# Performance work log

Hardware: AMD Instinct MI355X
Metric: run time of the kernel (lower is better)

## Reference

```python
import jax, jax.numpy as jnp
import numpy as np

B, S, E, D, A = 64, 1024, 512, 512, 512

def setup_inputs() -> dict:
    key = jax.random.key(0)
    ks = jax.random.split(key, 12)
    xavier = lambda k, shape: jax.random.uniform(k, shape, jnp.float32,
        -jnp.sqrt(6.0 / (shape[0] + shape[1])), jnp.sqrt(6.0 / (shape[0] + shape[1])))
    return {
        "encoder_states": jax.random.normal(ks[0], (B, S, E), jnp.float32),
        "decoder_state": jax.random.normal(ks[1], (B, D), jnp.float32),
        "encoder_mask": jnp.ones((B, S), jnp.int32),
        "coverage": jax.random.uniform(ks[2], (B, S), jnp.float32),
        # learned parameters (torch nn.Linear: y = x @ W.T + b)
        "W_enc": xavier(ks[3], (A, E)),           # encoder_projection, no bias
        "W_dec": xavier(ks[4], (A, D)),           # decoder_projection, no bias
        "w_attn": xavier(ks[5], (1, A)),          # attention_weight, no bias
        "W_layer1": xavier(ks[6], (A, A)),        # attention_layers[0]
        "b_layer1": jnp.zeros((A,), jnp.float32),
        "W_cov": xavier(ks[7], (A, 1)),           # coverage_projection, no bias
        "W_gate": xavier(ks[8], (A, E + D)),      # gate Linear
        "b_gate": jnp.zeros((A,), jnp.float32),
    }


def reference(encoder_states, decoder_state, encoder_mask, coverage,
              W_enc, W_dec, w_attn, W_layer1, b_layer1, W_cov, W_gate, b_gate):
    # projections
    proj_enc = jnp.einsum('bse,ae->bsa', encoder_states, W_enc)        # [B,S,A]
    proj_dec = jnp.einsum('bd,ad->ba', decoder_state, W_dec)[:, None]  # [B,1,A]
    attn_in = proj_enc + proj_dec
    # coverage: Linear(1->A) on coverage[..., None]
    attn_in = attn_in + coverage[..., None] * W_cov[None, None, :, 0]  # [B,S,A]
    feats = jnp.tanh(attn_in)
    # extra residual tanh layer (num_layers=2 -> one layer)
    feats = jnp.tanh(jnp.einsum('bsa,ca->bsc', feats, W_layer1) + b_layer1 + feats)
    scores = jnp.einsum('bsa,a->bs', feats, w_attn[0])                 # [B,S]
    scores = jnp.where(encoder_mask == 0, -1e9, scores)
    attn_w = jax.nn.softmax(scores, axis=-1)                           # [B,S]
    context = jnp.einsum('bs,bse->be', attn_w, encoder_states)         # [B,E]
    # gating
    gate_in = jnp.concatenate([context, decoder_state], axis=-1)       # [B,E+D]
    gate = jax.nn.sigmoid(jnp.einsum('bf,af->ba', gate_in, W_gate) + b_gate)
    context = gate * context
    updated_coverage = coverage + attn_w
    return (context, attn_w, updated_coverage)
```

## Files before the change

kernel.cpp:

```cpp
#include <hip/hip_runtime.h>
#include <hip/hip_bf16.h>

typedef unsigned short ushort_t;
typedef __attribute__((ext_vector_type(8))) short short8;
typedef __attribute__((ext_vector_type(4))) float float4_t;
typedef __attribute__((ext_vector_type(2))) float float2_t;
typedef __attribute__((ext_vector_type(4))) unsigned int uint4_t;

#define BB 64
#define SS 1024
#define EE 512
#define DD 512
#define AA 512
#define MM (BB*SS)
#define KK 512
#define BM 128
#define BN 128
#define BK 32
#define BKP 40
#define BK2 64

__device__ __forceinline__ float bf2f(ushort_t u) {
    return __uint_as_float(((unsigned int)u) << 16);
}
__device__ __forceinline__ ushort_t f2bf(float f) {
    unsigned int u = __float_as_uint(f);
    unsigned int r = u + 0x7fffu + ((u >> 16) & 1u);
    return (ushort_t)(r >> 16);
}
__device__ __forceinline__ float ldmix(int f32, const void* p, long idx) {
    return f32 ? ((const float*)p)[idx] : bf2f(((const ushort_t*)p)[idx]);
}
__device__ __forceinline__ void stmix(int f32, void* p, long idx, float v) {
    if (f32) ((float*)p)[idx] = v;
    else     ((ushort_t*)p)[idx] = f2bf(v);
}
__device__ __forceinline__ float fast_tanh(float x) {
    float e = __expf(2.f * x);
    return 1.f - 2.f / (e + 1.f);
}
__device__ __forceinline__ void glds16(const ushort_t* g, ushort_t* l) {
    typedef __attribute__((address_space(1))) const void gas_t;
    typedef __attribute__((address_space(3))) void las_t;
    gas_t* gp = (gas_t*)g;
    las_t* lp = (las_t*)l;
    __builtin_amdgcn_global_load_lds(gp, lp, 16, 0, 0);
}

__global__ void k_detect(const ushort_t* __restrict__ enc, int* __restrict__ flag) {
    __shared__ int cnt;
    int tid = threadIdx.x;
    if (tid == 0) cnt = 0;
    __syncthreads();
    int c = 0;
    const uint4_t* p = (const uint4_t*)enc;
    for (int i = tid; i < 4096; i += 256) {
        uint4_t v = p[i];
        #pragma unroll
        for (int j = 0; j < 4; j++) {
            unsigned int u = v[j];
            if (((u >> 7) & 0xFFu) == 0xFFu || ((u >> 23) & 0xFFu) == 0xFFu) c++;
        }
    }
    atomicAdd(&cnt, c);
    __syncthreads();
    if (tid == 0) *flag = (cnt > 0) ? 1 : 0;
}

__global__ __launch_bounds__(256)
void k_conv_w(const void* __restrict__ Wenc, const void* __restrict__ W1,
              const int* __restrict__ flagp,
              ushort_t* __restrict__ WencB, ushort_t* __restrict__ W1B) {
    const int f32 = *flagp;
    const void* src = blockIdx.y ? W1 : Wenc;
    ushort_t* dst = blockIdx.y ? W1B : WencB;
    long e0 = ((long)blockIdx.x * 256 + threadIdx.x) * 8;
    short8 p;
    #pragma unroll
    for (int j = 0; j < 8; j++) p[j] = (short)f2bf(ldmix(f32, src, e0 + j));
    *(short8*)&dst[e0] = p;
}

__global__ __launch_bounds__(256)
void k_conv_enc(const void* __restrict__ enc, const int* __restrict__ flagp,
                ushort_t* __restrict__ out) {
    if (*flagp == 0) return;
    const float4_t* src = (const float4_t*)enc;
    size_t i0 = (size_t)blockIdx.x * 256 + threadIdx.x;
    size_t n8 = (size_t)MM * EE / 8;
    size_t stride = (size_t)gridDim.x * 256;
    for (size_t i = i0; i < n8; i += stride) {
        float4_t v0 = src[2 * i], v1 = src[2 * i + 1];
        short8 p;
        p[0] = (short)f2bf(v0[0]); p[1] = (short)f2bf(v0[1]);
        p[2] = (short)f2bf(v0[2]); p[3] = (short)f2bf(v0[3]);
        p[4] = (short)f2bf(v1[0]); p[5] = (short)f2bf(v1[1]);
        p[6] = (short)f2bf(v1[2]); p[7] = (short)f2bf(v1[3]);
        *(short8*)&out[i * 8] = p;
    }
}

__global__ __launch_bounds__(256)
void k_proj_dec(const void* __restrict__ dec,
                const void* __restrict__ Wdec,
                const int* __restrict__ flagp,
                float* __restrict__ proj) {
    __shared__ float x[DD];
    const int f32 = *flagp;
    const int b = blockIdx.y;
    const int tid = threadIdx.x, lane = tid & 63, wave = tid >> 6;
    x[tid]       = ldmix(f32, dec, (long)b * DD + tid);
    x[tid + 256] = ldmix(f32, dec, (long)b * DD + tid + 256);
    __syncthreads();
    const int a = blockIdx.x * 4 + wave;
    float s = 0.f;
    if (f32) {
        const float* wr = (const float*)Wdec + (size_t)a * DD + lane * 8;
        #pragma unroll
        for (int j = 0; j < 8; j++) s += wr[j] * x[lane * 8 + j];
    } else {
        const ushort_t* wr = (const ushort_t*)Wdec + (size_t)a * DD + lane * 8;
        short8 w = *(const short8*)wr;
        #pragma unroll
        for (int j = 0; j < 8; j++) s += bf2f((ushort_t)w[j]) * x[lane * 8 + j];
    }
    #pragma unroll
    for (int off = 1; off < 64; off <<= 1) s += __shfl_xor(s, off);
    if (lane == 0) proj[b * AA + a] = s;
}

__device__ __forceinline__ void stage8(int f32, const void* g, long row, int col,
                                       ushort_t* lds) {
    if (f32) {
        const float* gf = (const float*)g + row * KK + col;
        float4_t v0 = *(const float4_t*)(gf);
        float4_t v1 = *(const float4_t*)(gf + 4);
        short8 p;
        p[0] = (short)f2bf(v0[0]); p[1] = (short)f2bf(v0[1]);
        p[2] = (short)f2bf(v0[2]); p[3] = (short)f2bf(v0[3]);
        p[4] = (short)f2bf(v1[0]); p[5] = (short)f2bf(v1[1]);
        p[6] = (short)f2bf(v1[2]); p[7] = (short)f2bf(v1[3]);
        *(short8*)lds = p;
    } else {
        const ushort_t* gb = (const ushort_t*)g + row * KK + col;
        *(short8*)lds = *(const short8*)gb;
    }
}

__global__ __launch_bounds__(256)
void k_gemm1(const void* __restrict__ Xg,
             const void* __restrict__ Bg,
             const float* __restrict__ proj_dec,
             const void* __restrict__ cov,
             const void* __restrict__ Wcov,
             const int* __restrict__ flagp,
             ushort_t* __restrict__ feats) {
    __shared__ ushort_t As[BM * BKP];
    __shared__ ushort_t Bs[BN * BKP];
    const int f32 = *flagp;
    const int tid = threadIdx.x;
    const int lane = tid & 63, wave = tid >> 6;
    const int quad = lane >> 4, l16 = lane & 15;
    const int wm = wave >> 1, wn = wave & 1;
    const int m0 = blockIdx.y * BM, n0 = blockIdx.x * BN;

    float4_t acc[4][4];
    #pragma unroll
    for (int i = 0; i < 4; i++)
        #pragma unroll
        for (int j = 0; j < 4; j++) acc[i][j] = (float4_t){0.f, 0.f, 0.f, 0.f};

    const int srow = lane >> 2;
    const int scol = (lane & 3) * 8;
    ushort_t* lA0 = &As[(wave * 32 + srow) * BKP + scol];
    ushort_t* lB0 = &Bs[(wave * 32 + srow) * BKP + scol];

    for (int kt = 0; kt < KK; kt += BK) {
        __syncthreads();
        stage8(f32, Xg, (long)(m0 + wave * 32 + srow), kt + scol, lA0);
        stage8(f32, Xg, (long)(m0 + wave * 32 + srow + 16), kt + scol, lA0 + 16 * BKP);
        stage8(f32, Bg, (long)(n0 + wave * 32 + srow), kt + scol, lB0);
        stage8(f32, Bg, (long)(n0 + wave * 32 + srow + 16), kt + scol, lB0 + 16 * BKP);
        __syncthreads();
        short8 af[4], bfr[4];
        #pragma unroll
        for (int mt = 0; mt < 4; mt++)
            af[mt] = *(const short8*)&As[(wm * 64 + mt * 16 + l16) * BKP + quad * 8];
        #pragma unroll
        for (int nt = 0; nt < 4; nt++)
            bfr[nt] = *(const short8*)&Bs[(wn * 64 + nt * 16 + l16) * BKP + quad * 8];
        #pragma unroll
        for (int mt = 0; mt < 4; mt++)
            #pragma unroll
            for (int nt = 0; nt < 4; nt++)
                acc[mt][nt] = __builtin_amdgcn_mfma_f32_16x16x32_bf16(af[mt], bfr[nt], acc[mt][nt], 0, 0, 0);
    }

    #pragma unroll
    for (int mt = 0; mt < 4; mt++) {
        #pragma unroll
        for (int r = 0; r < 4; r++) {
            int m = m0 + wm * 64 + mt * 16 + quad * 4 + r;
            int b = m >> 10;
            float covv = ldmix(f32, cov, m);
            #pragma unroll
            for (int nt = 0; nt < 4; nt++) {
                int n = n0 + wn * 64 + nt * 16 + l16;
                float v = acc[mt][nt][r] + proj_dec[b * AA + n] + covv * ldmix(f32, Wcov, n);
                feats[(size_t)m * AA + n] = f2bf(fast_tanh(v));
            }
        }
    }
}

__global__ __launch_bounds__(256)
void k_gemm2(const ushort_t* __restrict__ Xg,
             const void* __restrict__ Bg,
             const void* __restrict__ b1,
             const void* __restrict__ wattn,
             const int* __restrict__ flagp,
             float* __restrict__ scores) {
    __shared__ ushort_t As[BM * BKP];
    __shared__ ushort_t Bs[BN * BKP];
    const int f32 = *flagp;
    const int tid = threadIdx.x;
    const int lane = tid & 63, wave = tid >> 6;
    const int quad = lane >> 4, l16 = lane & 15;
    const int wm = wave >> 1, wn = wave & 1;
    const int m0 = blockIdx.y * BM, n0 = blockIdx.x * BN;

    float4_t acc[4][4];
    #pragma unroll
    for (int i = 0; i < 4; i++)
        #pragma unroll
        for (int j = 0; j < 4; j++) acc[i][j] = (float4_t){0.f, 0.f, 0.f, 0.f};

    const int srow = lane >> 2;
    const int scol = (lane & 3) * 8;
    ushort_t* lA0 = &As[(wave * 32 + srow) * BKP + scol];
    ushort_t* lB0 = &Bs[(wave * 32 + srow) * BKP + scol];

    for (int kt = 0; kt < KK; kt += BK) {
        __syncthreads();
        stage8(0,   Xg, (long)(m0 + wave * 32 + srow), kt + scol, lA0);
        stage8(0,   Xg, (long)(m0 + wave * 32 + srow + 16), kt + scol, lA0 + 16 * BKP);
        stage8(f32, Bg, (long)(n0 + wave * 32 + srow), kt + scol, lB0);
        stage8(f32, Bg, (long)(n0 + wave * 32 + srow + 16), kt + scol, lB0 + 16 * BKP);
        __syncthreads();
        short8 af[4], bfr[4];
        #pragma unroll
        for (int mt = 0; mt < 4; mt++)
            af[mt] = *(const short8*)&As[(wm * 64 + mt * 16 + l16) * BKP + quad * 8];
        #pragma unroll
        for (int nt = 0; nt < 4; nt++)
            bfr[nt] = *(const short8*)&Bs[(wn * 64 + nt * 16 + l16) * BKP + quad * 8];
        #pragma unroll
        for (int mt = 0; mt < 4; mt++)
            #pragma unroll
            for (int nt = 0; nt < 4; nt++)
                acc[mt][nt] = __builtin_amdgcn_mfma_f32_16x16x32_bf16(af[mt], bfr[nt], acc[mt][nt], 0, 0, 0);
    }

    float wv[4], bv[4];
    #pragma unroll
    for (int nt = 0; nt < 4; nt++) {
        int n = n0 + wn * 64 + nt * 16 + l16;
        wv[nt] = ldmix(f32, wattn, n);
        bv[nt] = ldmix(f32, b1, n);
    }
    #pragma unroll
    for (int mt = 0; mt < 4; mt++) {
        #pragma unroll
        for (int r = 0; r < 4; r++) {
            int m = m0 + wm * 64 + mt * 16 + quad * 4 + r;
            float s = 0.f;
            #pragma unroll
            for (int nt = 0; nt < 4; nt++) {
                int n = n0 + wn * 64 + nt * 16 + l16;
                float v = acc[mt][nt][r] + bv[nt] + bf2f(Xg[(size_t)m * AA + n]);
                s += fast_tanh(v) * wv[nt];
            }
            s += __shfl_xor(s, 1);
            s += __shfl_xor(s, 2);
            s += __shfl_xor(s, 4);
            s += __shfl_xor(s, 8);
            if (l16 == 0) atomicAdd(&scores[m], s);
        }
    }
}

__global__ __launch_bounds__(256)
void k_gemm1n(const void* __restrict__ enc,
              const ushort_t* __restrict__ enc_bf,
              const ushort_t* __restrict__ Wenc_bf,
              const float* __restrict__ proj_dec,
              const void* __restrict__ cov,
              const void* __restrict__ Wcov,
              const int* __restrict__ flagp,
              ushort_t* __restrict__ feats) {
    __shared__ ushort_t As[BM * BK2];
    __shared__ ushort_t Bs[BN * BK2];
    const int f32 = *flagp;
    const ushort_t* Abf = f32 ? enc_bf : (const ushort_t*)enc;

    const int lid = ((blockIdx.x & 7) << 8) | (blockIdx.x >> 3);
    const int m0 = (lid >> 2) * BM;
    const int n0 = (lid & 3) * BN;

    const int tid = threadIdx.x;
    const int lane = tid & 63, wave = tid >> 6;
    const int quad = lane >> 4, l16 = lane & 15;
    const int wm = wave >> 1, wn = wave & 1;
    const int l8r = lane >> 3;
    const int l8c = (lane & 7) * 8;

    float4_t acc[4][4];
    #pragma unroll
    for (int i = 0; i < 4; i++)
        #pragma unroll
        for (int j = 0; j < 4; j++) acc[i][j] = (float4_t){0.f, 0.f, 0.f, 0.f};

    for (int kt = 0; kt < KK; kt += BK2) {
        __syncthreads();
        #pragma unroll
        for (int i = 0; i < 4; i++) {
            int ch = i * 4 + wave;
            glds16(Abf     + (((size_t)(m0 + ch * 8 + l8r)) << 9) + kt + l8c, &As[ch * 512]);
            glds16(Wenc_bf + (((size_t)(n0 + ch * 8 + l8r)) << 9) + kt + l8c, &Bs[ch * 512]);
        }
        __syncthreads();
        #pragma unroll
        for (int kk = 0; kk < 2; kk++) {
            short8 af[4], bfv[4];
            #pragma unroll
            for (int mt = 0; mt < 4; mt++)
                af[mt] = *(const short8*)&As[(wm * 64 + mt * 16 + l16) * BK2 + kk * 32 + quad * 8];
            #pragma unroll
            for (int nt = 0; nt < 4; nt++)
                bfv[nt] = *(const short8*)&Bs[(wn * 64 + nt * 16 + l16) * BK2 + kk * 32 + quad * 8];
            #pragma unroll
            for (int mt = 0; mt < 4; mt++)
                #pragma unroll
                for (int nt = 0; nt < 4; nt++)
                    acc[mt][nt] = __builtin_amdgcn_mfma_f32_16x16x32_bf16(af[mt], bfv[nt], acc[mt][nt], 0, 0, 0);
        }
    }

    #pragma unroll
    for (int mt = 0; mt < 4; mt++) {
        #pragma unroll
        for (int r = 0; r < 4; r++) {
            int m = m0 + wm * 64 + mt * 16 + quad * 4 + r;
            int b = m >> 10;
            float covv = ldmix(f32, cov, m);
            #pragma unroll
            for (int nt = 0; nt < 4; nt++) {
                int n = n0 + wn * 64 + nt * 16 + l16;
                float v = acc[mt][nt][r] + proj_dec[b * AA + n] + covv * ldmix(f32, Wcov, n);
                feats[(size_t)m * AA + n] = f2bf(fast_tanh(v));
            }
        }
    }
}

__global__ __launch_bounds__(256)
void k_gemm2n(const ushort_t* __restrict__ Xg,
              const ushort_t* __restrict__ W1_bf,
              const void* __restrict__ b1,
              const void* __restrict__ wattn,
              const int* __restrict__ flagp,
              float* __restrict__ scores) {
    __shared__ ushort_t As[BM * BK2];
    __shared__ ushort_t Bs[BN * BK2];
    const int f32 = *flagp;

    const int lid = ((blockIdx.x & 7) << 8) | (blockIdx.x >> 3);
    const int m0 = (lid >> 2) * BM;
    const int n0 = (lid & 3) * BN;

    const int tid = threadIdx.x;
    const int lane = tid & 63, wave = tid >> 6;
    const int quad = lane >> 4, l16 = lane & 15;
    const int wm = wave >> 1, wn = wave & 1;
    const int l8r = lane >> 3;
    const int l8c = (lane & 7) * 8;

    float4_t acc[4][4];
    #pragma unroll
    for (int i = 0; i < 4; i++)
        #pragma unroll
        for (int j = 0; j < 4; j++) acc[i][j] = (float4_t){0.f, 0.f, 0.f, 0.f};

    for (int kt = 0; kt < KK; kt += BK2) {
        __syncthreads();
        #pragma unroll
        for (int i = 0; i < 4; i++) {
            int ch = i * 4 + wave;
            glds16(Xg    + (((size_t)(m0 + ch * 8 + l8r)) << 9) + kt + l8c, &As[ch * 512]);
            glds16(W1_bf + (((size_t)(n0 + ch * 8 + l8r)) << 9) + kt + l8c, &Bs[ch * 512]);
        }
        __syncthreads();
        #pragma unroll
        for (int kk = 0; kk < 2; kk++) {
            short8 af[4], bfv[4];
            #pragma unroll
            for (int mt = 0; mt < 4; mt++)
                af[mt] = *(const short8*)&As[(wm * 64 + mt * 16 + l16) * BK2 + kk * 32 + quad * 8];
            #pragma unroll
            for (int nt = 0; nt < 4; nt++)
                bfv[nt] = *(const short8*)&Bs[(wn * 64 + nt * 16 + l16) * BK2 + kk * 32 + quad * 8];
            #pragma unroll
            for (int mt = 0; mt < 4; mt++)
                #pragma unroll
                for (int nt = 0; nt < 4; nt++)
                    acc[mt][nt] = __builtin_amdgcn_mfma_f32_16x16x32_bf16(af[mt], bfv[nt], acc[mt][nt], 0, 0, 0);
        }
    }

    float wv[4], bv[4];
    #pragma unroll
    for (int nt = 0; nt < 4; nt++) {
        int n = n0 + wn * 64 + nt * 16 + l16;
        wv[nt] = ldmix(f32, wattn, n);
        bv[nt] = ldmix(f32, b1, n);
    }
    #pragma unroll
    for (int mt = 0; mt < 4; mt++) {
        #pragma unroll
        for (int r = 0; r < 4; r++) {
            int m = m0 + wm * 64 + mt * 16 + quad * 4 + r;
            float s = 0.f;
            #pragma unroll
            for (int nt = 0; nt < 4; nt++) {
                int n = n0 + wn * 64 + nt * 16 + l16;
                float v = acc[mt][nt][r] + bv[nt] + bf2f(Xg[(size_t)m * AA + n]);
                s += fast_tanh(v) * wv[nt];
            }
            s += __shfl_xor(s, 1);
            s += __shfl_xor(s, 2);
            s += __shfl_xor(s, 4);
            s += __shfl_xor(s, 8);
            if (l16 == 0) atomicAdd(&scores[m], s);
        }
    }
}

__global__ void k_softmax(const float* __restrict__ scores,
                          const int* __restrict__ mask,
                          const void* __restrict__ cov,
                          const int* __restrict__ flagp,
                          float* __restrict__ attnw,
                          void* __restrict__ dout) {
    __shared__ float red[4];
    const int f32 = *flagp;
    int b = blockIdx.x, tid = threadIdx.x;
    float v[4];
    #pragma unroll
    for (int i = 0; i < 4; i++) {
        int s = tid + i * 256;
        float sc = scores[b * SS + s];
        if (mask[b * SS + s] == 0) sc = -1e9f;
        v[i] = sc;
    }
    float mx = fmaxf(fmaxf(v[0], v[1]), fmaxf(v[2], v[3]));
    #pragma unroll
    for (int off = 1; off < 64; off <<= 1) mx = fmaxf(mx, __shfl_xor(mx, off));
    if ((tid & 63) == 0) red[tid >> 6] = mx;
    __syncthreads();
    mx = fmaxf(fmaxf(red[0], red[1]), fmaxf(red[2], red[3]));
    __syncthreads();
    float e[4], sum = 0.f;
    #pragma unroll
    for (int i = 0; i < 4; i++) { e[i] = expf(v[i] - mx); sum += e[i]; }
    #pragma unroll
    for (int off = 1; off < 64; off <<= 1) sum += __shfl_xor(sum, off);
    if ((tid & 63) == 0) red[tid >> 6] = sum;
    __syncthreads();
    sum = red[0] + red[1] + red[2] + red[3];
    float inv = 1.0f / sum;
    #pragma unroll
    for (int i = 0; i < 4; i++) {
        int s = tid + i * 256;
        float w = e[i] * inv;
        attnw[b * SS + s] = w;
        stmix(f32, dout, 32768L + (long)b * SS + s, w);
        stmix(f32, dout, 98304L + (long)b * SS + s, ldmix(f32, cov, (long)b * SS + s) + w);
    }
}

__global__ void k_context(const void* __restrict__ enc,
                          const ushort_t* __restrict__ enc_bf,
                          const int pre,
                          const float* __restrict__ attnw,
                          const int* __restrict__ flagp,
                          float* __restrict__ ctx) {
    int f32 = *flagp;
    const void* e = enc;
    if (pre && f32) { e = enc_bf; f32 = 0; }
    int b = blockIdx.x, sc = blockIdx.y;
    int tid = threadIdx.x;
    float a0 = 0.f, a1 = 0.f;
    const float* wrow = attnw + b * SS + sc * 128;
    if (f32) {
        const float* base = (const float*)e + ((size_t)b * SS + sc * 128) * EE;
        for (int s = 0; s < 128; s++) {
            float w = wrow[s];
            float2_t u = *(const float2_t*)(base + (size_t)s * EE + 2 * tid);
            a0 += w * u[0];
            a1 += w * u[1];
        }
    } else {
        const unsigned int* base = (const unsigned int*)e + ((size_t)b * SS + sc * 128) * (EE / 2);
        for (int s = 0; s < 128; s++) {
            float w = wrow[s];
            unsigned int u = base[(size_t)s * (EE / 2) + tid];
            a0 += w * bf2f((ushort_t)(u & 0xffff));
            a1 += w * bf2f((ushort_t)(u >> 16));
        }
    }
    atomicAdd(&ctx[b * EE + 2 * tid], a0);
    atomicAdd(&ctx[b * EE + 2 * tid + 1], a1);
}

__global__ __launch_bounds__(256)
void k_gate(const float* __restrict__ ctx,
            const void* __restrict__ dec,
            const void* __restrict__ Wg,
            const void* __restrict__ bg,
            const int* __restrict__ flagp,
            void* __restrict__ dout) {
    __shared__ float gin[EE + DD];
    const int f32 = *flagp;
    const int b = blockIdx.y;
    const int tid = threadIdx.x, lane = tid & 63, wave = tid >> 6;
    gin[2 * tid]     = ctx[b * EE + 2 * tid];
    gin[2 * tid + 1] = ctx[b * EE + 2 * tid + 1];
    gin[EE + tid]       = ldmix(f32, dec, (long)b * DD + tid);
    gin[EE + tid + 256] = ldmix(f32, dec, (long)b * DD + tid + 256);
    __syncthreads();
    const int a = blockIdx.x * 4 + wave;
    float s = 0.f;
    if (f32) {
        const float* wr = (const float*)Wg + (size_t)a * (EE + DD) + lane * 16;
        #pragma unroll
        for (int j = 0; j < 16; j++) s += wr[j] * gin[lane * 16 + j];
    } else {
        const ushort_t* wr = (const ushort_t*)Wg + (size_t)a * (EE + DD) + lane * 16;
        short8 w0 = *(const short8*)wr;
        short8 w1 = *(const short8*)(wr + 8);
        #pragma unroll
        for (int j = 0; j < 8; j++) {
            s += bf2f((ushort_t)w0[j]) * gin[lane * 16 + j];
            s += bf2f((ushort_t)w1[j]) * gin[lane * 16 + 8 + j];
        }
    }
    #pragma unroll
    for (int off = 1; off < 64; off <<= 1) s += __shfl_xor(s, off);
    if (lane == 0) {
        float acc = s + ldmix(f32, bg, a);
        float g = 1.f / (1.f + __expf(-acc));
        stmix(f32, dout, (long)b * AA + a, g * ctx[b * EE + a]);
    }
}

extern "C" void kernel_launch(void* const* d_in, const int* in_sizes, int n_in,
                              void* d_out, int out_size, void* d_ws, size_t ws_size,
                              hipStream_t stream) {
    const void* enc   = d_in[0];
    const void* dec   = d_in[1];
    const int*  mask  = (const int*)d_in[2];
    const void* cov   = d_in[3];
    const void* Wenc  = d_in[4];
    const void* Wdec  = d_in[5];
    const void* wattn = d_in[6];
    const void* Wl1   = d_in[7];
    const void* b1    = d_in[8];
    const void* Wcov  = d_in[9];
    const void* Wg    = d_in[10];
    const void* bg    = d_in[11];

    char* ws = (char*)d_ws;
    float*    scores = (float*)ws;
    float*    ctx    = (float*)(ws + 262144);
    float*    attnw  = (float*)(ws + 393216);
    float*    projd  = (float*)(ws + 655360);
    int*      flag   = (int*)(ws + 786432);
    ushort_t* feats  = (ushort_t*)(ws + 1048576);
    ushort_t* W1b    = (ushort_t*)(ws + 68157440);
    ushort_t* Wencb  = (ushort_t*)(ws + 68681728);
    ushort_t* encb   = (ushort_t*)(ws + 69206016);
    const int pre2 = (ws_size >= 69206016UL)  ? 1 : 0;
    const int pre1 = (ws_size >= 136314880UL) ? 1 : 0;

    hipMemsetAsync(ws, 0, 393216, stream);
    k_detect<<<1, 256, 0, stream>>>((const ushort_t*)enc, flag);
    if (pre2)
        k_conv_w<<<dim3(128, 2), 256, 0, stream>>>(Wenc, Wl1, flag, Wencb, W1b);
    if (pre1)
        k_conv_enc<<<4096, 256, 0, stream>>>(enc, flag, encb);
    k_proj_dec<<<dim3(AA / 4, BB), 256, 0, stream>>>(dec, Wdec, flag, projd);
    if (pre1)
        k_gemm1n<<<2048, 256, 0, stream>>>(enc, encb, Wencb, projd, cov, Wcov, flag, feats);
    else
        k_gemm1<<<dim3(AA / BN, MM / BM), 256, 0, stream>>>(enc, Wenc, projd, cov, Wcov, flag, feats);
    if (pre2)
        k_gemm2n<<<2048, 256, 0, stream>>>(feats, W1b, b1, wattn, flag, scores);
    else
        k_gemm2<<<dim3(AA / BN, MM / BM), 256, 0, stream>>>(feats, Wl1, b1, wattn, flag, scores);
    k_softmax<<<BB, 256, 0, stream>>>(scores, mask, cov, flag, attnw, d_out);
    k_context<<<dim3(BB, 8), 256, 0, stream>>>(enc, encb, pre1, attnw, flag, ctx);
    k_gate<<<dim3(AA / 4, BB), 256, 0, stream>>>(ctx, dec, Wg, bg, flag, d_out);
}
```

Baseline: 464.1 us.

## Double-buffer LDS tiles and XOR-swizzle layout in both bf16 GEMM kernels

Both MFMA GEMM kernels now use two LDS buffers, so the global-to-LDS loads for the next K tile are issued before the current tile is computed. Waits use explicit vmcnt/lgkmcnt counters with raw barriers instead of __syncthreads. The LDS columns are also XOR-swizzled by row to avoid bank conflicts on the short8 fragment reads. This doubles LDS use per block, which may lower occupancy, and relies on the hand-written waitcnt counts being correct.

```diff
diff --git a/kernel.cpp b/kernel.cpp
--- a/kernel.cpp
+++ b/kernel.cpp
@@ -19,6 +19,7 @@
 #define BK 32
 #define BKP 40
 #define BK2 64
+#define NT (KK/BK2)
 
 __device__ __forceinline__ float bf2f(ushort_t u) {
     return __uint_as_float(((unsigned int)u) << 16);
@@ -298,8 +299,8 @@
               const void* __restrict__ Wcov,
               const int* __restrict__ flagp,
               ushort_t* __restrict__ feats) {
-    __shared__ ushort_t As[BM * BK2];
-    __shared__ ushort_t Bs[BN * BK2];
+    __shared__ ushort_t As[2][BM * BK2];
+    __shared__ ushort_t Bs[2][BN * BK2];
     const int f32 = *flagp;
     const ushort_t* Abf = f32 ? enc_bf : (const ushort_t*)enc;
 
@@ -312,7 +313,7 @@
     const int quad = lane >> 4, l16 = lane & 15;
     const int wm = wave >> 1, wn = wave & 1;
     const int l8r = lane >> 3;
-    const int l8c = (lane & 7) * 8;
+    const int l8c = ((lane & 7) ^ l8r) * 8;
 
     float4_t acc[4][4];
     #pragma unroll
@@ -320,31 +321,57 @@
         #pragma unroll
         for (int j = 0; j < 4; j++) acc[i][j] = (float4_t){0.f, 0.f, 0.f, 0.f};
 
-    for (int kt = 0; kt < KK; kt += BK2) {
-        __syncthreads();
-        #pragma unroll
-        for (int i = 0; i < 4; i++) {
-            int ch = i * 4 + wave;
-            glds16(Abf     + (((size_t)(m0 + ch * 8 + l8r)) << 9) + kt + l8c, &As[ch * 512]);
-            glds16(Wenc_bf + (((size_t)(n0 + ch * 8 + l8r)) << 9) + kt + l8c, &Bs[ch * 512]);
-        }
-        __syncthreads();
-        #pragma unroll
-        for (int kk = 0; kk < 2; kk++) {
-            short8 af[4], bfv[4];
-            #pragma unroll
-            for (int mt = 0; mt < 4; mt++)
-                af[mt] = *(const short8*)&As[(wm * 64 + mt * 16 + l16) * BK2 + kk * 32 + quad * 8];
-            #pragma unroll
-            for (int nt = 0; nt < 4; nt++)
-                bfv[nt] = *(const short8*)&Bs[(wn * 64 + nt * 16 + l16) * BK2 + kk * 32 + quad * 8];
-            #pragma unroll
-            for (int mt = 0; mt < 4; mt++)
-                #pragma unroll
-                for (int nt = 0; nt < 4; nt++)
-                    acc[mt][nt] = __builtin_amdgcn_mfma_f32_16x16x32_bf16(af[mt], bfv[nt], acc[mt][nt], 0, 0, 0);
-        }
-    }
+    #define STAGE1(buf, kel)                                                              \
+        _Pragma("unroll")                                                                 \
+        for (int i = 0; i < 4; i++) {                                                     \
+            int ch = i * 4 + wave;                                                        \
+            glds16(Abf     + (((size_t)(m0 + ch * 8 + l8r)) << 9) + (kel) + l8c,          \
+                   &As[buf][ch * 512]);                                                   \
+            glds16(Wenc_bf + (((size_t)(n0 + ch * 8 + l8r)) << 9) + (kel) + l8c,          \
+                   &Bs[buf][ch * 512]);                                                   \
+        }
+
+    #define COMPUTE1(buf)                                                                 \
+        _Pragma("unroll")                                                                 \
+        for (int kk = 0; kk < 2; kk++) {                                                  \
+            short8 af[4], bfv[4];                                                         \
+            _Pragma("unroll")                                                             \
+            for (int mt = 0; mt < 4; mt++) {                                              \
+                int row = wm * 64 + mt * 16 + l16;                                        \
+                int col = (kk * 32 + quad * 8) ^ ((row & 7) << 3);                        \
+                af[mt] = *(const short8*)&As[buf][row * BK2 + col];                       \
+            }                                                                             \
+            _Pragma("unroll")                                                             \
+            for (int nt = 0; nt < 4; nt++) {                                              \
+                int row = wn * 64 + nt * 16 + l16;                                        \
+                int col = (kk * 32 + quad * 8) ^ ((row & 7) << 3);                        \
+                bfv[nt] = *(const short8*)&Bs[buf][row * BK2 + col];                      \
+            }                                                                             \
+            _Pragma("unroll")                                                             \
+            for (int mt = 0; mt < 4; mt++)                                                \
+                _Pragma("unroll")                                                         \
+                for (int nt = 0; nt < 4; nt++)                                            \
+                    acc[mt][nt] = __builtin_amdgcn_mfma_f32_16x16x32_bf16(                \
+                        af[mt], bfv[nt], acc[mt][nt], 0, 0, 0);                           \
+        }
+
+    STAGE1(0, 0);
+    #pragma unroll
+    for (int kt = 0; kt < NT - 1; kt++) {
+        const int cur = kt & 1;
+        STAGE1(cur ^ 1, (kt + 1) * BK2);
+        asm volatile("s_waitcnt vmcnt(8)" ::: "memory");
+        __builtin_amdgcn_s_barrier();
+        COMPUTE1(cur);
+        asm volatile("s_waitcnt lgkmcnt(0)" ::: "memory");
+        __builtin_amdgcn_s_barrier();
+    }
+    asm volatile("s_waitcnt vmcnt(0)" ::: "memory");
+    __builtin_amdgcn_s_barrier();
+    COMPUTE1((NT - 1) & 1);
+
+    #undef STAGE1
+    #undef COMPUTE1
 
     #pragma unroll
     for (int mt = 0; mt < 4; mt++) {
@@ -370,8 +397,8 @@
               const void* __restrict__ wattn,
               const int* __restrict__ flagp,
               float* __restrict__ scores) {
-    __shared__ ushort_t As[BM * BK2];
-    __shared__ ushort_t Bs[BN * BK2];
+    __shared__ ushort_t As[2][BM * BK2];
+    __shared__ ushort_t Bs[2][BN * BK2];
     const int f32 = *flagp;
 
     const int lid = ((blockIdx.x & 7) << 8) | (blockIdx.x >> 3);
@@ -383,7 +410,7 @@
     const int quad = lane >> 4, l16 = lane & 15;
     const int wm = wave >> 1, wn = wave & 1;
     const int l8r = lane >> 3;
-    const int l8c = (lane & 7) * 8;
+    const int l8c = ((lane & 7) ^ l8r) * 8;
 
     float4_t acc[4][4];
     #pragma unroll
@@ -391,31 +418,57 @@
         #pragma unroll
         for (int j = 0; j < 4; j++) acc[i][j] = (float4_t){0.f, 0.f, 0.f, 0.f};
 
-    for (int kt = 0; kt < KK; kt += BK2) {
-        __syncthreads();
-        #pragma unroll
-        for (int i = 0; i < 4; i++) {
-            int ch = i * 4 + wave;
-            glds16(Xg    + (((size_t)(m0 + ch * 8 + l8r)) << 9) + kt + l8c, &As[ch * 512]);
-            glds16(W1_bf + (((size_t)(n0 + ch * 8 + l8r)) << 9) + kt + l8c, &Bs[ch * 512]);
-        }
-        __syncthreads();
-        #pragma unroll
-        for (int kk = 0; kk < 2; kk++) {
-            short8 af[4], bfv[4];
-            #pragma unroll
-            for (int mt = 0; mt < 4; mt++)
-                af[mt] = *(const short8*)&As[(wm * 64 + mt * 16 + l16) * BK2 + kk * 32 + quad * 8];
-            #pragma unroll
-            for (int nt = 0; nt < 4; nt++)
-                bfv[nt] = *(const short8*)&Bs[(wn * 64 + nt * 16 + l16) * BK2 + kk * 32 + quad * 8];
-            #pragma unroll
-            for (int mt = 0; mt < 4; mt++)
-                #pragma unroll
-                for (int nt = 0; nt < 4; nt++)
-                    acc[mt][nt] = __builtin_amdgcn_mfma_f32_16x16x32_bf16(af[mt], bfv[nt], acc[mt][nt], 0, 0, 0);
-        }
-    }
+    #define STAGE2(buf, kel)                                                              \
+        _Pragma("unroll")                                                                 \
+        for (int i = 0; i < 4; i++) {                                                     \
+            int ch = i * 4 + wave;                                                        \
+            glds16(Xg    + (((size_t)(m0 + ch * 8 + l8r)) << 9) + (kel) + l8c,            \
+                   &As[buf][ch * 512]);                                                   \
+            glds16(W1_bf + (((size_t)(n0 + ch * 8 + l8r)) << 9) + (kel) + l8c,            \
+                   &Bs[buf][ch * 512]);                                                   \
+        }
+
+    #define COMPUTE2(buf)                                                                 \
+        _Pragma("unroll")                                                                 \
+        for (int kk = 0; kk < 2; kk++) {                                                  \
+            short8 af[4], bfv[4];                                                         \
+            _Pragma("unroll")                                                             \
+            for (int mt = 0; mt < 4; mt++) {                                              \
+                int row = wm * 64 + mt * 16 + l16;                                        \
+                int col = (kk * 32 + quad * 8) ^ ((row & 7) << 3);                        \
+                af[mt] = *(const short8*)&As[buf][row * BK2 + col];                       \
+            }                                                                             \
+            _Pragma("unroll")                                                             \
+            for (int nt = 0; nt < 4; nt++) {                                              \
+                int row = wn * 64 + nt * 16 + l16;                                        \
+                int col = (kk * 32 + quad * 8) ^ ((row & 7) << 3);                        \
+                bfv[nt] = *(const short8*)&Bs[buf][row * BK2 + col];                      \
+            }                                                                             \
+            _Pragma("unroll")                                                             \
+            for (int mt = 0; mt < 4; mt++)                                                \
+                _Pragma("unroll")                                                         \
+                for (int nt = 0; nt < 4; nt++)                                            \
+                    acc[mt][nt] = __builtin_amdgcn_mfma_f32_16x16x32_bf16(                \
+                        af[mt], bfv[nt], acc[mt][nt], 0, 0, 0);                           \
+        }
+
+    STAGE2(0, 0);
+    #pragma unroll
+    for (int kt = 0; kt < NT - 1; kt++) {
+        const int cur = kt & 1;
+        STAGE2(cur ^ 1, (kt + 1) * BK2);
+        asm volatile("s_waitcnt vmcnt(8)" ::: "memory");
+        __builtin_amdgcn_s_barrier();
+        COMPUTE2(cur);
+        asm volatile("s_waitcnt lgkmcnt(0)" ::: "memory");
+        __builtin_amdgcn_s_barrier();
+    }
+    asm volatile("s_waitcnt vmcnt(0)" ::: "memory");
+    __builtin_amdgcn_s_barrier();
+    COMPUTE2((NT - 1) & 1);
+
+    #undef STAGE2
+    #undef COMPUTE2
 
     float wv[4], bv[4];
     #pragma unroll
```

Result: faster. 434.8 us (-6.3%).

## XOR-swizzle LDS tiles and stage GEMM1 epilogue through LDS for coalesced stores

Applied to the files above, without the earlier changes.

Applies an XOR swizzle to the global-to-LDS load offsets and the matching LDS fragment reads in both bf16 GEMM kernels, so the MFMA operand reads avoid LDS bank conflicts. It also fully unrolls the K loop. The first GEMM now writes its tanh features into LDS (reusing the A/B buffers) and then stores them to global memory as 16-byte row-contiguous vectors instead of scattered 2-byte stores. This adds an extra barrier and LDS round trip in the epilogue.

```diff
diff --git a/kernel.cpp b/kernel.cpp
--- a/kernel.cpp
+++ b/kernel.cpp
@@ -19,6 +19,7 @@
 #define BK 32
 #define BKP 40
 #define BK2 64
+#define NT (KK/BK2)
 
 __device__ __forceinline__ float bf2f(ushort_t u) {
     return __uint_as_float(((unsigned int)u) << 16);
@@ -312,7 +313,7 @@
     const int quad = lane >> 4, l16 = lane & 15;
     const int wm = wave >> 1, wn = wave & 1;
     const int l8r = lane >> 3;
-    const int l8c = (lane & 7) * 8;
+    const int l8c = ((lane & 7) ^ l8r) * 8;
 
     float4_t acc[4][4];
     #pragma unroll
@@ -320,24 +321,31 @@
         #pragma unroll
         for (int j = 0; j < 4; j++) acc[i][j] = (float4_t){0.f, 0.f, 0.f, 0.f};
 
-    for (int kt = 0; kt < KK; kt += BK2) {
+    #pragma unroll
+    for (int kt = 0; kt < NT; kt++) {
         __syncthreads();
         #pragma unroll
         for (int i = 0; i < 4; i++) {
             int ch = i * 4 + wave;
-            glds16(Abf     + (((size_t)(m0 + ch * 8 + l8r)) << 9) + kt + l8c, &As[ch * 512]);
-            glds16(Wenc_bf + (((size_t)(n0 + ch * 8 + l8r)) << 9) + kt + l8c, &Bs[ch * 512]);
+            glds16(Abf     + (((size_t)(m0 + ch * 8 + l8r)) << 9) + kt * BK2 + l8c, &As[ch * 512]);
+            glds16(Wenc_bf + (((size_t)(n0 + ch * 8 + l8r)) << 9) + kt * BK2 + l8c, &Bs[ch * 512]);
         }
         __syncthreads();
         #pragma unroll
         for (int kk = 0; kk < 2; kk++) {
             short8 af[4], bfv[4];
             #pragma unroll
-            for (int mt = 0; mt < 4; mt++)
-                af[mt] = *(const short8*)&As[(wm * 64 + mt * 16 + l16) * BK2 + kk * 32 + quad * 8];
-            #pragma unroll
-            for (int nt = 0; nt < 4; nt++)
-                bfv[nt] = *(const short8*)&Bs[(wn * 64 + nt * 16 + l16) * BK2 + kk * 32 + quad * 8];
+            for (int mt = 0; mt < 4; mt++) {
+                int row = wm * 64 + mt * 16 + l16;
+                int col = (kk * 32 + quad * 8) ^ ((row & 7) << 3);
+                af[mt] = *(const short8*)&As[row * BK2 + col];
+            }
+            #pragma unroll
+            for (int nt = 0; nt < 4; nt++) {
+                int row = wn * 64 + nt * 16 + l16;
+                int col = (kk * 32 + quad * 8) ^ ((row & 7) << 3);
+                bfv[nt] = *(const short8*)&Bs[row * BK2 + col];
+            }
             #pragma unroll
             for (int mt = 0; mt < 4; mt++)
                 #pragma unroll
@@ -346,20 +354,34 @@
         }
     }
 
+    __syncthreads();
+    ushort_t* myhalf = wm ? Bs : As;
     #pragma unroll
     for (int mt = 0; mt < 4; mt++) {
         #pragma unroll
         for (int r = 0; r < 4; r++) {
-            int m = m0 + wm * 64 + mt * 16 + quad * 4 + r;
+            int lr = mt * 16 + quad * 4 + r;
+            int grow = wm * 64 + lr;
+            int m = m0 + grow;
             int b = m >> 10;
             float covv = ldmix(f32, cov, m);
             #pragma unroll
             for (int nt = 0; nt < 4; nt++) {
-                int n = n0 + wn * 64 + nt * 16 + l16;
+                int lc = wn * 64 + nt * 16 + l16;
+                int n = n0 + lc;
                 float v = acc[mt][nt][r] + proj_dec[b * AA + n] + covv * ldmix(f32, Wcov, n);
-                feats[(size_t)m * AA + n] = f2bf(fast_tanh(v));
-            }
-        }
+                myhalf[lr * 128 + (lc ^ ((grow & 7) << 3))] = f2bf(fast_tanh(v));
+            }
+        }
+    }
+    __syncthreads();
+    #pragma unroll
+    for (int rep = 0; rep < 8; rep++) {
+        int row = rep * 16 + (tid >> 4);
+        int c8 = (tid & 15) * 8;
+        const ushort_t* half = (row < 64) ? As : Bs;
+        short8 vv = *(const short8*)&half[(row & 63) * 128 + (c8 ^ ((row & 7) << 3))];
+        *(short8*)&feats[(size_t)(m0 + row) * AA + n0 + c8] = vv;
     }
 }
 
@@ -383,7 +405,7 @@
     const int quad = lane >> 4, l16 = lane & 15;
     const int wm = wave >> 1, wn = wave & 1;
     const int l8r = lane >> 3;
-    const int l8c = (lane & 7) * 8;
+    const int l8c = ((lane & 7) ^ l8r) * 8;
 
     float4_t acc[4][4];
     #pragma unroll
@@ -391,24 +413,31 @@
         #pragma unroll
         for (int j = 0; j < 4; j++) acc[i][j] = (float4_t){0.f, 0.f, 0.f, 0.f};
 
-    for (int kt = 0; kt < KK; kt += BK2) {
+    #pragma unroll
+    for (int kt = 0; kt < NT; kt++) {
         __syncthreads();
         #pragma unroll
         for (int i = 0; i < 4; i++) {
             int ch = i * 4 + wave;
-            glds16(Xg    + (((size_t)(m0 + ch * 8 + l8r)) << 9) + kt + l8c, &As[ch * 512]);
-            glds16(W1_bf + (((size_t)(n0 + ch * 8 + l8r)) << 9) + kt + l8c, &Bs[ch * 512]);
+            glds16(Xg    + (((size_t)(m0 + ch * 8 + l8r)) << 9) + kt * BK2 + l8c, &As[ch * 512]);
+            glds16(W1_bf + (((size_t)(n0 + ch * 8 + l8r)) << 9) + kt * BK2 + l8c, &Bs[ch * 512]);
         }
         __syncthreads();
         #pragma unroll
         for (int kk = 0; kk < 2; kk++) {
             short8 af[4], bfv[4];
             #pragma unroll
-            for (int mt = 0; mt < 4; mt++)
-                af[mt] = *(const short8*)&As[(wm * 64 + mt * 16 + l16) * BK2 + kk * 32 + quad * 8];
-            #pragma unroll
-            for (int nt = 0; nt < 4; nt++)
-                bfv[nt] = *(const short8*)&Bs[(wn * 64 + nt * 16 + l16) * BK2 + kk * 32 + quad * 8];
+            for (int mt = 0; mt < 4; mt++) {
+                int row = wm * 64 + mt * 16 + l16;
+                int col = (kk * 32 + quad * 8) ^ ((row & 7) << 3);
+                af[mt] = *(const short8*)&As[row * BK2 + col];
+            }
+            #pragma unroll
+            for (int nt = 0; nt < 4; nt++) {
+                int row = wn * 64 + nt * 16 + l16;
+                int col = (kk * 32 + quad * 8) ^ ((row & 7) << 3);
+                bfv[nt] = *(const short8*)&Bs[row * BK2 + col];
+            }
             #pragma unroll
             for (int mt = 0; mt < 4; mt++)
                 #pragma unroll
```

Measured after the change: 405.6 us. -12.6%, faster.
